# Kernel tuning notes

Hardware: AMD Instinct MI355X
Metric: run time of the kernel (lower is better)

The kernel has to match this reference:

```python
import jax, jax.numpy as jnp
import numpy as np

K = 16
NUM_CLASSES = 1000
TAU = 0.2
LOGIT_SCALE = 20.0


def setup_inputs() -> dict:
    key = jax.random.key(0)
    k1, k2, k3, k4, k5 = jax.random.split(key, 5)
    B, D, N = 2048, 256, 100000
    x = jax.random.normal(k1, (B, D), dtype=jnp.float32)
    mean = jax.random.normal(k2, (D,), dtype=jnp.float32)
    std = jax.random.uniform(k3, (D,), dtype=jnp.float32, minval=0.5, maxval=1.5)
    mem_features = jax.random.normal(k4, (N, D), dtype=jnp.float32)
    mem_labels = jax.random.randint(k5, (N,), 0, NUM_CLASSES)
    return {"x": x, "mean": mean, "std": std,
            "mem_features": mem_features, "mem_labels": mem_labels}


def reference(x, mean, std, mem_features, mem_labels):
    # preprocess: standardize then L2-normalize rows (eval mode, no noise)
    x = (x - mean) / std
    norm = jnp.maximum(jnp.linalg.norm(x, axis=1, keepdims=True), 1e-6)
    x = x / norm
    # dense cosine similarity: [B, N]
    sims = jnp.einsum('bd,nd->bn', x, mem_features)
    # top-k neighbors per query
    top_sims, top_idx = jax.lax.top_k(sims, K)          # [B, K]
    top_lbl = mem_labels[top_idx]                       # [B, K]
    weights = jax.nn.softmax(top_sims / max(1e-6, TAU), axis=1)
    # scatter-add softmax weights into class logits
    B = x.shape[0]
    rows = jnp.arange(B)[:, None]                       # [B, 1]
    logits = jnp.zeros((B, NUM_CLASSES), dtype=x.dtype).at[rows, top_lbl].add(weights)
    return logits * LOGIT_SCALE
```

## Files before the change

### kernel.cpp

```cpp
#include <hip/hip_runtime.h>
#include <math.h>

constexpr int BQ   = 2048;
constexpr int D    = 256;
constexpr int NMEM = 100000;
constexpr int TOPK = 16;
constexpr int NCLS = 1000;
constexpr float TAU = 0.2f;
constexpr float LOGIT_SCALE = 20.0f;

constexpr int KTOT = 256;
constexpr int BK   = 64;
constexpr int TM   = 128;
constexpr int TN   = 128;
constexpr int CTILES = 17;
constexpr int CHUNK  = TN * CTILES;
constexpr int NCH    = 48;
constexpr int RBLK   = BQ / TM;
constexpr int NBLK   = RBLK * NCH;
constexpr int TOTAL_IT = CTILES * (KTOT / BK);
constexpr float XSCALE = 16.0f;
constexpr float INV_XS = 0.0625f;
constexpr float THR    = 3.0f;
constexpr float THRS   = 48.0f;
constexpr int CAP    = 512;
constexpr int MSEL   = 64;
constexpr int SELCAP = 96;
constexpr float NEG  = -3.0e38f;

using i32x4  = __attribute__((ext_vector_type(4))) int;
using i32x8  = __attribute__((ext_vector_type(8))) int;
using f32x16 = __attribute__((ext_vector_type(16))) float;

__device__ __forceinline__ unsigned f2e4m3(float f) {
    const unsigned u = __float_as_uint(f);
    const unsigned s = (u >> 24) & 0x80u;
    const int e = (int)((u >> 23) & 0xff);
    int te = e - 120;
    if (te <= 0) return s;
    const unsigned m = u & 0x7fffffu;
    const unsigned r = m + 0x7ffffu + ((m >> 20) & 1u);
    unsigned keep;
    if (r & 0x800000u) { ++te; keep = 0; } else keep = (r >> 20) & 7u;
    if (te >= 16 || (te == 15 && keep == 7)) return s | 0x7eu;
    return s | ((unsigned)te << 3) | keep;
}

__device__ __forceinline__ void load_lds16(const void* g, void* l) {
    __builtin_amdgcn_global_load_lds((const __attribute__((address_space(1))) void*)g,
                                     (__attribute__((address_space(3))) void*)l,
                                     16, 0, 0);
}

__global__ __launch_bounds__(256) void knn_prep(
    const float* __restrict__ x, const float* __restrict__ mean,
    const float* __restrict__ stdv, unsigned char* __restrict__ A1,
    float* __restrict__ XN, int* __restrict__ cnt)
{
    const int row = blockIdx.x;
    const int t = threadIdx.x;
    float v = (x[row * D + t] - mean[t]) / stdv[t];
    float s = v * v;
    #pragma unroll
    for (int off = 32; off > 0; off >>= 1) s += __shfl_down(s, off, 64);
    __shared__ float wsum[4];
    __shared__ float nrm;
    const int lane = t & 63, wid = t >> 6;
    if (lane == 0) wsum[wid] = s;
    __syncthreads();
    if (t == 0) {
        nrm = fmaxf(sqrtf(wsum[0] + wsum[1] + wsum[2] + wsum[3]), 1e-6f);
        cnt[row] = 0;
    }
    __syncthreads();
    const float xnv = v / nrm;
    A1[(size_t)row * KTOT + t] = (unsigned char)f2e4m3(xnv * XSCALE);
    XN[(size_t)row * D + t] = xnv;
}

__global__ __launch_bounds__(256) void knn_convb(
    const float* __restrict__ mem, unsigned char* __restrict__ B1)
{
    const int tid = threadIdx.x;
    const int rloc = tid >> 5, t = tid & 31;
    const long n = (long)blockIdx.x * 8 + rloc;
    if (n >= NMEM) return;
    const float* src = mem + n * D + t * 8;
    const float4 v0 = *(const float4*)(src);
    const float4 v1 = *(const float4*)(src + 4);
    const float f[8] = {v0.x, v0.y, v0.z, v0.w, v1.x, v1.y, v1.z, v1.w};
    unsigned long long pk = 0;
    #pragma unroll
    for (int i = 0; i < 8; ++i)
        pk |= (unsigned long long)f2e4m3(f[i]) << (8 * i);
    *(unsigned long long*)(B1 + n * KTOT + t * 8) = pk;
}

__global__ __launch_bounds__(256, 3) void knn_gemm_topk(
    const unsigned char* __restrict__ A1, const unsigned char* __restrict__ B1,
    int* __restrict__ cnt, uint2* __restrict__ cand_buf)
{
    __shared__ alignas(16) unsigned char As[3][TM * BK];
    __shared__ alignas(16) unsigned char Bs[3][TN * BK];

    const int tid  = threadIdx.x;
    const int lane = tid & 63, wave = tid >> 6;
    const int wm = wave >> 1, wn = wave & 1;
    const int l31 = lane & 31;
    const int kb  = lane >> 5;

    const int nblk = blockIdx.x;
    const int xcd = nblk & 7, bi = nblk >> 3;
    const int rb = bi & 15;
    const int ch = (bi >> 4) + 6 * xcd;
    const int row0  = rb * TM;
    const int cbase = ch * CHUNK;

    int aoff[2][2], boff[2][2];
    #pragma unroll
    for (int ti = 0; ti < 2; ++ti) {
        const int ar = wm * 64 + ti * 32 + l31;
        const int br = wn * 64 + ti * 32 + l31;
        #pragma unroll
        for (int c = 0; c < 2; ++c) {
            aoff[ti][c] = ar * BK + (((2 * kb + c) - (ar >> 1)) & 3) * 16;
            boff[ti][c] = br * BK + (((2 * kb + c) - (br >> 1)) & 3) * 16;
        }
    }

    const unsigned char* aSrc[2];
    int cSub[2], bSeg[2];
    #pragma unroll
    for (int s = 0; s < 2; ++s) {
        const int ci = s * 256 + tid;
        const int r = ci >> 2, sl = ci & 3;
        aSrc[s] = A1 + (size_t)(row0 + r) * KTOT + (((sl + (r >> 1)) & 3) << 4);
        cSub[s] = r;
        bSeg[s] = ((sl + (r >> 1)) & 3) << 4;
    }
    const unsigned char* bB[2];
    auto computeBB = [&](int tile) {
        #pragma unroll
        for (int s = 0; s < 2; ++s) {
            int candi = cbase + tile * TN + cSub[s];
            if (candi >= NMEM) candi = NMEM - 1;
            bB[s] = B1 + (size_t)candi * KTOT + bSeg[s];
        }
    };
    auto stage = [&](int buf, int kofs) {
        #pragma unroll
        for (int s = 0; s < 2; ++s)
            load_lds16(aSrc[s] + kofs, (char*)As[buf] + s * 4096 + wave * 1024);
        #pragma unroll
        for (int s = 0; s < 2; ++s)
            load_lds16(bB[s] + kofs, (char*)Bs[buf] + s * 4096 + wave * 1024);
    };

    f32x16 acc[2][2];
    #pragma unroll
    for (int i = 0; i < 2; ++i)
        #pragma unroll
        for (int j = 0; j < 2; ++j)
            #pragma unroll
            for (int r = 0; r < 16; ++r) acc[i][j][r] = 0.f;

    computeBB(0);
    stage(0, 0);
    stage(1, 64);
    asm volatile("s_waitcnt vmcnt(4)" ::: "memory");
    __builtin_amdgcn_sched_barrier(0);
    __builtin_amdgcn_s_barrier();

    int p = 0;
    for (int it = 0; it < TOTAL_IT; ++it) {
        const unsigned char* Ab = As[p];
        const unsigned char* Bb = Bs[p];
        i32x8 Afr[2], Bfr[2];
        #pragma unroll
        for (int ti = 0; ti < 2; ++ti) {
            const i32x4 alo = *(const i32x4*)(Ab + aoff[ti][0]);
            const i32x4 ahi = *(const i32x4*)(Ab + aoff[ti][1]);
            Afr[ti] = __builtin_shufflevector(alo, ahi, 0, 1, 2, 3, 4, 5, 6, 7);
            const i32x4 blo = *(const i32x4*)(Bb + boff[ti][0]);
            const i32x4 bhi = *(const i32x4*)(Bb + boff[ti][1]);
            Bfr[ti] = __builtin_shufflevector(blo, bhi, 0, 1, 2, 3, 4, 5, 6, 7);
        }

        const int is = it + 2;
        const bool have2 = (is < TOTAL_IT);
        if (have2) {
            if ((is & 3) == 0) computeBB(is >> 2);
            int pn = p + 2; if (pn >= 3) pn -= 3;
            stage(pn, (is & 3) << 6);
        }

        #pragma unroll
        for (int ti = 0; ti < 2; ++ti)
            #pragma unroll
            for (int tj = 0; tj < 2; ++tj)
                acc[ti][tj] = __builtin_amdgcn_mfma_scale_f32_32x32x64_f8f6f4(
                    Afr[ti], Bfr[tj], acc[ti][tj], 0, 0,
                    0, 0x7f7f7f7f, 0, 0x7f7f7f7f);

        if ((it & 3) == 3) {
            const int t = it >> 2;
            const int tb = cbase + t * TN;
            #pragma unroll
            for (int ti = 0; ti < 2; ++ti) {
                const int rb0 = row0 + wm * 64 + ti * 32 + 4 * kb;
                #pragma unroll
                for (int tj = 0; tj < 2; ++tj) {
                    const int cidx = tb + wn * 64 + tj * 32 + l31;
                    #pragma unroll
                    for (int r = 0; r < 16; ++r) {
                        const float v = acc[ti][tj][r];
                        if (v > THRS && cidx < NMEM) {
                            const int rg = rb0 + (r & 3) + 8 * (r >> 2);
                            const int pos = atomicAdd(&cnt[rg], 1);
                            if (pos < CAP)
                                cand_buf[(size_t)rg * CAP + pos] =
                                    make_uint2(__float_as_uint(v * INV_XS),
                                               (unsigned)cidx);
                        }
                        acc[ti][tj][r] = 0.f;
                    }
                }
            }
        }

        if (it < TOTAL_IT - 1) {
            if (have2) {
                asm volatile("s_waitcnt vmcnt(4)" ::: "memory");
            } else {
                asm volatile("s_waitcnt vmcnt(0)" ::: "memory");
            }
            __builtin_amdgcn_sched_barrier(0);
            __builtin_amdgcn_s_barrier();
        }
        ++p; if (p >= 3) p = 0;
    }
}

__global__ __launch_bounds__(256) void knn_final(
    const int* __restrict__ cnt, const uint2* __restrict__ cand_buf,
    const float* __restrict__ xn, const float* __restrict__ mem,
    const int* __restrict__ labels, float* __restrict__ out)
{
    constexpr float BSCALE = 200.0f;
    __shared__ float cls[NCLS];
    __shared__ uint2 cl[CAP];
    __shared__ int   hist[1024];
    __shared__ int   psum[256];
    __shared__ float tstar;
    __shared__ int   scount;
    __shared__ int   seli[SELCAP];
    __shared__ float ex[SELCAP];
    __shared__ float fs[TOPK];
    __shared__ int   fi[TOPK];
    __shared__ float zshare;

    const int row = blockIdx.x;
    const int tid = threadIdx.x;
    const int lane = tid & 63, w = tid >> 6;

    const float4 xr = *(const float4*)(xn + (size_t)row * D + lane * 4);

    for (int c = tid; c < NCLS; c += 256) cls[c] = 0.f;
    for (int i = tid; i < 1024; i += 256) hist[i] = 0;
    int n = cnt[row]; if (n > CAP) n = CAP;
    for (int i = tid; i < n; i += 256) cl[i] = cand_buf[(size_t)row * CAP + i];
    if (tid == 0) scount = 0;
    __syncthreads();

    for (int i = tid; i < n; i += 256) {
        const float v = __uint_as_float(cl[i].x);
        int b = (int)((v - THR) * BSCALE);
        b = max(0, min(1023, b));
        atomicAdd(&hist[b], 1);
    }
    __syncthreads();
    psum[tid] = hist[4 * tid] + hist[4 * tid + 1] + hist[4 * tid + 2] + hist[4 * tid + 3];
    __syncthreads();
    if (tid == 0) {
        int cum = 0, g = 255;
        for (; g >= 0; --g) {
            if (cum + psum[g] >= MSEL) break;
            cum += psum[g];
        }
        float t = THR;
        if (g >= 0) {
            int bb = 4 * g + 3;
            for (; bb > 4 * g; --bb) {
                cum += hist[bb];
                if (cum >= MSEL) break;
            }
            if (bb == 4 * g) cum += hist[bb];
            t = THR + (float)bb * (1.0f / BSCALE);
        }
        tstar = t;
    }
    __syncthreads();
    for (int i = tid; i < n; i += 256) {
        const float v = __uint_as_float(cl[i].x);
        if (v >= tstar) {
            const int p = atomicAdd(&scount, 1);
            if (p < SELCAP) seli[p] = (int)cl[i].y;
        }
    }
    __syncthreads();
    int ns = scount; if (ns > SELCAP) ns = SELCAP;

    for (int c = w; c < ns; c += 4) {
        const float4 mv = *(const float4*)(mem + (size_t)seli[c] * D + lane * 4);
        float s = xr.x * mv.x + xr.y * mv.y + xr.z * mv.z + xr.w * mv.w;
        #pragma unroll
        for (int off = 32; off > 0; off >>= 1) s += __shfl_down(s, off, 64);
        if (lane == 0) ex[c] = s;
    }
    __syncthreads();

    if (tid == 0) {
        float kmin = NEG; int kslot = 0;
        #pragma unroll
        for (int s = 0; s < TOPK; ++s) { fs[s] = NEG; fi[s] = -1; }
        for (int c = 0; c < ns; ++c) {
            const float v = ex[c];
            if (v > kmin) {
                fs[kslot] = v; fi[kslot] = seli[c];
                kmin = fs[0]; kslot = 0;
                #pragma unroll
                for (int s = 1; s < TOPK; ++s) {
                    const float tq = fs[s];
                    if (tq < kmin) { kmin = tq; kslot = s; }
                }
            }
        }
        float smax = fs[0];
        #pragma unroll
        for (int s = 1; s < TOPK; ++s) smax = fmaxf(smax, fs[s]);
        float e[TOPK]; float Z = 0.f;
        #pragma unroll
        for (int s = 0; s < TOPK; ++s) {
            e[s] = (fi[s] >= 0) ? expf((fs[s] - smax) * (1.0f / TAU)) : 0.f;
            Z += e[s];
        }
        for (int s = 0; s < TOPK; ++s) {
            if (fi[s] >= 0) cls[labels[fi[s]]] += e[s];
        }
        zshare = Z;
    }
    __syncthreads();
    const float scale = LOGIT_SCALE / zshare;
    for (int c = tid; c < NCLS; c += 256)
        out[(size_t)row * NCLS + c] = cls[c] * scale;
}

extern "C" void kernel_launch(void* const* d_in, const int* in_sizes, int n_in,
                              void* d_out, int out_size, void* d_ws, size_t ws_size,
                              hipStream_t stream) {
    (void)in_sizes; (void)n_in; (void)out_size; (void)ws_size;
    const float* x    = (const float*)d_in[0];
    const float* mean = (const float*)d_in[1];
    const float* stdv = (const float*)d_in[2];
    const float* mem  = (const float*)d_in[3];
    const int*   lbl  = (const int*)d_in[4];
    float* out = (float*)d_out;

    unsigned char* A1 = (unsigned char*)d_ws;
    float* XN = (float*)(A1 + (size_t)BQ * KTOT);
    unsigned char* B1 = (unsigned char*)(XN + (size_t)BQ * D);
    int* cnt = (int*)(B1 + (size_t)NMEM * KTOT);
    uint2* cand = (uint2*)(cnt + BQ);

    knn_prep<<<BQ, 256, 0, stream>>>(x, mean, stdv, A1, XN, cnt);
    knn_convb<<<(NMEM + 7) / 8, 256, 0, stream>>>(mem, B1);
    knn_gemm_topk<<<NBLK, 256, 0, stream>>>(A1, B1, cnt, cand);
    knn_final<<<BQ, 256, 0, stream>>>(cnt, cand, XN, mem, lbl, out);
}
```

Measured before the change: 369.8 us.

## Keep query A tile resident in registers instead of restaging through LDS

The query block's FP8 A fragments (128 rows x 256 K) are loaded once into registers at kernel start and reused across all 17 candidate tiles. Previously they were re-fetched from global into LDS and read back on every K step. This removes half the LDS staging traffic and the matching global loads and LDS reads per iteration. The loop is restructured to tile by K-step, with B-only staging and adjusted vmcnt waits. The cost is 64 extra VGPRs per thread for Areg, which may pressure occupancy under launch_bounds(256,3), though LDS usage drops.

```diff
diff --git a/kernel.cpp b/kernel.cpp
--- a/kernel.cpp
+++ b/kernel.cpp
@@ -100,7 +100,6 @@
     const unsigned char* __restrict__ A1, const unsigned char* __restrict__ B1,
     int* __restrict__ cnt, uint2* __restrict__ cand_buf)
 {
-    __shared__ alignas(16) unsigned char As[3][TM * BK];
     __shared__ alignas(16) unsigned char Bs[3][TN * BK];
 
     const int tid  = threadIdx.x;
@@ -116,25 +115,33 @@
     const int row0  = rb * TM;
     const int cbase = ch * CHUNK;
 
-    int aoff[2][2], boff[2][2];
+    i32x8 Areg[2][4];
     #pragma unroll
     for (int ti = 0; ti < 2; ++ti) {
-        const int ar = wm * 64 + ti * 32 + l31;
-        const int br = wn * 64 + ti * 32 + l31;
-        #pragma unroll
-        for (int c = 0; c < 2; ++c) {
-            aoff[ti][c] = ar * BK + (((2 * kb + c) - (ar >> 1)) & 3) * 16;
-            boff[ti][c] = br * BK + (((2 * kb + c) - (br >> 1)) & 3) * 16;
-        }
-    }
-
-    const unsigned char* aSrc[2];
+        const unsigned char* ar =
+            A1 + (size_t)(row0 + wm * 64 + ti * 32 + l31) * KTOT + kb * 32;
+        #pragma unroll
+        for (int ks = 0; ks < 4; ++ks) {
+            const i32x4 lo = *(const i32x4*)(ar + ks * 64);
+            const i32x4 hi = *(const i32x4*)(ar + ks * 64 + 16);
+            Areg[ti][ks] = __builtin_shufflevector(lo, hi, 0, 1, 2, 3, 4, 5, 6, 7);
+        }
+    }
+
+    int boff[2][2];
+    #pragma unroll
+    for (int tj = 0; tj < 2; ++tj) {
+        const int br = wn * 64 + tj * 32 + l31;
+        #pragma unroll
+        for (int c = 0; c < 2; ++c)
+            boff[tj][c] = br * BK + (((2 * kb + c) - (br >> 1)) & 3) * 16;
+    }
+
     int cSub[2], bSeg[2];
     #pragma unroll
     for (int s = 0; s < 2; ++s) {
         const int ci = s * 256 + tid;
         const int r = ci >> 2, sl = ci & 3;
-        aSrc[s] = A1 + (size_t)(row0 + r) * KTOT + (((sl + (r >> 1)) & 3) << 4);
         cSub[s] = r;
         bSeg[s] = ((sl + (r >> 1)) & 3) << 4;
     }
@@ -147,10 +154,7 @@
             bB[s] = B1 + (size_t)candi * KTOT + bSeg[s];
         }
     };
-    auto stage = [&](int buf, int kofs) {
-        #pragma unroll
-        for (int s = 0; s < 2; ++s)
-            load_lds16(aSrc[s] + kofs, (char*)As[buf] + s * 4096 + wave * 1024);
+    auto stageB = [&](int buf, int kofs) {
         #pragma unroll
         for (int s = 0; s < 2; ++s)
             load_lds16(bB[s] + kofs, (char*)Bs[buf] + s * 4096 + wave * 1024);
@@ -165,79 +169,78 @@
             for (int r = 0; r < 16; ++r) acc[i][j][r] = 0.f;
 
     computeBB(0);
-    stage(0, 0);
-    stage(1, 64);
-    asm volatile("s_waitcnt vmcnt(4)" ::: "memory");
+    stageB(0, 0);
+    stageB(1, 64);
+    asm volatile("s_waitcnt vmcnt(2)" ::: "memory");
     __builtin_amdgcn_sched_barrier(0);
     __builtin_amdgcn_s_barrier();
 
     int p = 0;
-    for (int it = 0; it < TOTAL_IT; ++it) {
-        const unsigned char* Ab = As[p];
-        const unsigned char* Bb = Bs[p];
-        i32x8 Afr[2], Bfr[2];
-        #pragma unroll
-        for (int ti = 0; ti < 2; ++ti) {
-            const i32x4 alo = *(const i32x4*)(Ab + aoff[ti][0]);
-            const i32x4 ahi = *(const i32x4*)(Ab + aoff[ti][1]);
-            Afr[ti] = __builtin_shufflevector(alo, ahi, 0, 1, 2, 3, 4, 5, 6, 7);
-            const i32x4 blo = *(const i32x4*)(Bb + boff[ti][0]);
-            const i32x4 bhi = *(const i32x4*)(Bb + boff[ti][1]);
-            Bfr[ti] = __builtin_shufflevector(blo, bhi, 0, 1, 2, 3, 4, 5, 6, 7);
-        }
-
-        const int is = it + 2;
-        const bool have2 = (is < TOTAL_IT);
-        if (have2) {
-            if ((is & 3) == 0) computeBB(is >> 2);
-            int pn = p + 2; if (pn >= 3) pn -= 3;
-            stage(pn, (is & 3) << 6);
-        }
-
-        #pragma unroll
-        for (int ti = 0; ti < 2; ++ti)
+    for (int t = 0; t < CTILES; ++t) {
+        #pragma unroll
+        for (int ks = 0; ks < 4; ++ks) {
+            const int g = t * 4 + ks;
+
+            const unsigned char* Bb = Bs[p];
+            i32x8 Bfr[2];
             #pragma unroll
-            for (int tj = 0; tj < 2; ++tj)
-                acc[ti][tj] = __builtin_amdgcn_mfma_scale_f32_32x32x64_f8f6f4(
-                    Afr[ti], Bfr[tj], acc[ti][tj], 0, 0,
-                    0, 0x7f7f7f7f, 0, 0x7f7f7f7f);
-
-        if ((it & 3) == 3) {
-            const int t = it >> 2;
-            const int tb = cbase + t * TN;
+            for (int tj = 0; tj < 2; ++tj) {
+                const i32x4 blo = *(const i32x4*)(Bb + boff[tj][0]);
+                const i32x4 bhi = *(const i32x4*)(Bb + boff[tj][1]);
+                Bfr[tj] = __builtin_shufflevector(blo, bhi, 0, 1, 2, 3, 4, 5, 6, 7);
+            }
+
+            const bool have2 = (g + 2 < TOTAL_IT);
+            if (have2) {
+                if (ks == 2) computeBB(t + 1);
+                int pn = p + 2; if (pn >= 3) pn -= 3;
+                stageB(pn, ((ks + 2) & 3) << 6);
+            }
+
             #pragma unroll
-            for (int ti = 0; ti < 2; ++ti) {
-                const int rb0 = row0 + wm * 64 + ti * 32 + 4 * kb;
+            for (int ti = 0; ti < 2; ++ti)
                 #pragma unroll
-                for (int tj = 0; tj < 2; ++tj) {
-                    const int cidx = tb + wn * 64 + tj * 32 + l31;
+                for (int tj = 0; tj < 2; ++tj)
+                    acc[ti][tj] = __builtin_amdgcn_mfma_scale_f32_32x32x64_f8f6f4(
+                        Areg[ti][ks], Bfr[tj], acc[ti][tj], 0, 0,
+                        0, 0x7f7f7f7f, 0, 0x7f7f7f7f);
+
+            if (ks == 3) {
+                const int tb = cbase + t * TN;
+                #pragma unroll
+                for (int ti = 0; ti < 2; ++ti) {
+                    const int rb0 = row0 + wm * 64 + ti * 32 + 4 * kb;
                     #pragma unroll
-                    for (int r = 0; r < 16; ++r) {
-                        const float v = acc[ti][tj][r];
-                        if (v > THRS && cidx < NMEM) {
-                            const int rg = rb0 + (r & 3) + 8 * (r >> 2);
-                            const int pos = atomicAdd(&cnt[rg], 1);
-                            if (pos < CAP)
-                                cand_buf[(size_t)rg * CAP + pos] =
-                                    make_uint2(__float_as_uint(v * INV_XS),
-                                               (unsigned)cidx);
+                    for (int tj = 0; tj < 2; ++tj) {
+                        const int cidx = tb + wn * 64 + tj * 32 + l31;
+                        #pragma unroll
+                        for (int r = 0; r < 16; ++r) {
+                            const float v = acc[ti][tj][r];
+                            if (v > THRS && cidx < NMEM) {
+                                const int rg = rb0 + (r & 3) + 8 * (r >> 2);
+                                const int pos = atomicAdd(&cnt[rg], 1);
+                                if (pos < CAP)
+                                    cand_buf[(size_t)rg * CAP + pos] =
+                                        make_uint2(__float_as_uint(v * INV_XS),
+                                                   (unsigned)cidx);
+                            }
+                            acc[ti][tj][r] = 0.f;
                         }
-                        acc[ti][tj][r] = 0.f;
                     }
                 }
             }
-        }
-
-        if (it < TOTAL_IT - 1) {
-            if (have2) {
-                asm volatile("s_waitcnt vmcnt(4)" ::: "memory");
-            } else {
-                asm volatile("s_waitcnt vmcnt(0)" ::: "memory");
-            }
-            __builtin_amdgcn_sched_barrier(0);
-            __builtin_amdgcn_s_barrier();
-        }
-        ++p; if (p >= 3) p = 0;
+
+            if (g < TOTAL_IT - 1) {
+                if (have2) {
+                    asm volatile("s_waitcnt vmcnt(2)" ::: "memory");
+                } else {
+                    asm volatile("s_waitcnt vmcnt(0)" ::: "memory");
+                }
+                __builtin_amdgcn_sched_barrier(0);
+                __builtin_amdgcn_s_barrier();
+            }
+            ++p; if (p >= 3) p = 0;
+        }
     }
 }
 
```

Result: slower. 420.7 us (+13.7%).
